# Optimization experiments

Measured on AMD Instinct MI355X. Metric: run time of the kernel, lower is better.

Reference implementation:

```python
import jax, jax.numpy as jnp
import numpy as np

N = 50000      # nodes
K = 15         # k_max candidate neighbors per node
D = 128        # node_dim
H = 64         # hidden_dim
K_MIN = 2.0
K_MAX = 15.0
TAU = 0.5      # edge_tau
LAM = 1.0      # selector_lambda


def setup_inputs() -> dict:
    key = jax.random.key(0)
    ks = jax.random.split(key, 16)
    x = jax.random.normal(ks[0], (N, D), dtype=jnp.float32)
    src = jax.random.randint(ks[1], (N * K,), 0, N)
    dst = jnp.repeat(jnp.arange(N), K)  # edges grouped by dst, as the module requires
    edge_index = jnp.stack([src, dst]).astype(jnp.int64)
    edge_dist = jax.random.uniform(ks[2], (N * K,), dtype=jnp.float32)

    def lin(k, fin, fout):
        return jax.random.normal(k, (fin, fout), dtype=jnp.float32) / np.sqrt(fin)

    EIN = 2 * D + 1  # edge MLP input: [x_dst, x_src, dist]
    return {
        "x": x, "edge_index": edge_index, "edge_dist": edge_dist,
        "ew1": lin(ks[3], EIN, H), "eb1": jnp.zeros((H,), jnp.float32),
        "ew2": lin(ks[4], H, H),   "eb2": jnp.zeros((H,), jnp.float32),
        "ew3": lin(ks[5], H, 1),   "eb3": jnp.zeros((1,), jnp.float32),
        "dw1": lin(ks[6], D + 1, H), "db1": jnp.zeros((H,), jnp.float32),
        "dw2": lin(ks[7], H, H),     "db2": jnp.zeros((H,), jnp.float32),
        "dw3": lin(ks[8], H, 1),     "db3": jnp.zeros((1,), jnp.float32),
    }


def reference(x, edge_index, edge_dist, ew1, eb1, ew2, eb2, ew3, eb3,
              dw1, db1, dw2, db2, dw3, db3):
    src_mat = edge_index[0].reshape(N, K)              # (N, K)
    x_src = x[src_mat]                                 # gather: (N, K, D)
    x_dst = jnp.broadcast_to(x[:, None, :], (N, K, D))
    edge_feat = jnp.concatenate([x_dst, x_src, edge_dist.reshape(N, K, 1)], axis=-1)

    # edge MLP -> logits (eval mode: no gumbel-logistic noise)
    h = jax.nn.relu(edge_feat @ ew1 + eb1)
    h = jax.nn.relu(h @ ew2 + eb2)
    edge_logits = (h @ ew3 + eb3)[..., 0]              # (N, K)
    edge_energy = jax.nn.sigmoid(edge_logits / TAU)

    # degree MLP -> continuous k per node
    degree_hint = edge_energy.sum(axis=1, keepdims=True)
    g = jax.nn.relu(jnp.concatenate([x, degree_hint], axis=1) @ dw1 + db1)
    g = jax.nn.relu(g @ dw2 + db2)
    k_raw = (g @ dw3 + db3)[:, 0]
    k_cont = K_MIN + (K_MAX - K_MIN) * jax.nn.sigmoid(k_raw)  # (N,)

    # per-node descending sort + straight-through top-k gate
    perm = jnp.argsort(-edge_energy, axis=1)
    energy_sorted = jnp.take_along_axis(edge_energy, perm, axis=1)
    ranks = jnp.arange(1, K + 1, dtype=x.dtype)[None, :]
    gate_soft = jax.nn.sigmoid((k_cont[:, None] - ranks) / LAM)
    k_int = jnp.clip(jnp.round(k_cont), K_MIN, K_MAX)
    gate_hard = (ranks <= k_int[:, None]).astype(gate_soft.dtype)
    gate = gate_soft + jax.lax.stop_gradient(gate_hard - gate_soft)

    gated_sorted = energy_sorted * gate
    inv_perm = jnp.argsort(perm, axis=1)               # undo the sort
    edge_gate = jnp.take_along_axis(gate, inv_perm, axis=1)
    edge_weight = jnp.take_along_axis(gated_sorted, inv_perm, axis=1)

    denom = jnp.maximum(edge_weight.sum(axis=1, keepdims=True), 1e-12)
    edge_weight = edge_weight / denom
    return (edge_weight.reshape(-1), edge_gate.reshape(-1),
            edge_energy.reshape(-1), k_cont)
```

## Files before the change

kernel.cpp:

```cpp
#include <hip/hip_runtime.h>
#include <cmath>

#define NN 50000
#define KK 15
#define DD 128
#define HH 64
#define NKE (NN * KK)

__global__ __launch_bounds__(256) void kP(const float* __restrict__ x,
                                          const float* __restrict__ ew1,
                                          const float* __restrict__ dw1,
                                          float* __restrict__ ws) {
    int lane = threadIdx.x & 63;
    int wv = __builtin_amdgcn_readfirstlane((int)(threadIdx.x >> 6));
    int r0 = blockIdx.x * 32 + wv * 8;
    if (r0 >= NN) return;

    const float* W0 = ew1;
    const float* W1 = ew1 + DD * HH;
    const float* W2 = dw1;
    const float* xw = x + (size_t)r0 * DD;

    float a0[8], a1[8], a2[8];
#pragma unroll
    for (int r = 0; r < 8; ++r) { a0[r] = 0.f; a1[r] = 0.f; a2[r] = 0.f; }

#pragma unroll 1
    for (int i4 = 0; i4 < DD / 4; ++i4) {
        float w00 = W0[(i4 * 4 + 0) * HH + lane];
        float w01 = W0[(i4 * 4 + 1) * HH + lane];
        float w02 = W0[(i4 * 4 + 2) * HH + lane];
        float w03 = W0[(i4 * 4 + 3) * HH + lane];
        float w10 = W1[(i4 * 4 + 0) * HH + lane];
        float w11 = W1[(i4 * 4 + 1) * HH + lane];
        float w12 = W1[(i4 * 4 + 2) * HH + lane];
        float w13 = W1[(i4 * 4 + 3) * HH + lane];
        float w20 = W2[(i4 * 4 + 0) * HH + lane];
        float w21 = W2[(i4 * 4 + 1) * HH + lane];
        float w22 = W2[(i4 * 4 + 2) * HH + lane];
        float w23 = W2[(i4 * 4 + 3) * HH + lane];
#pragma unroll
        for (int r = 0; r < 8; ++r) {
            float4 xv = *(const float4*)(xw + r * DD + i4 * 4);
            a0[r] = fmaf(xv.x, w00, a0[r]);
            a0[r] = fmaf(xv.y, w01, a0[r]);
            a0[r] = fmaf(xv.z, w02, a0[r]);
            a0[r] = fmaf(xv.w, w03, a0[r]);
            a1[r] = fmaf(xv.x, w10, a1[r]);
            a1[r] = fmaf(xv.y, w11, a1[r]);
            a1[r] = fmaf(xv.z, w12, a1[r]);
            a1[r] = fmaf(xv.w, w13, a1[r]);
            a2[r] = fmaf(xv.x, w20, a2[r]);
            a2[r] = fmaf(xv.y, w21, a2[r]);
            a2[r] = fmaf(xv.z, w22, a2[r]);
            a2[r] = fmaf(xv.w, w23, a2[r]);
        }
    }
    float* o0 = ws + (size_t)r0 * HH + lane;
    float* o1 = ws + (size_t)NN * HH + (size_t)r0 * HH + lane;
    float* o2 = ws + 2 * (size_t)NN * HH + (size_t)r0 * HH + lane;
#pragma unroll
    for (int r = 0; r < 8; ++r) {
        o0[r * HH] = a0[r];
        o1[r * HH] = a1[r];
        o2[r * HH] = a2[r];
    }
}

__global__ __launch_bounds__(128, 4) void kE(const int* __restrict__ srcIdx,
                                             const float* __restrict__ dist,
                                             const float* __restrict__ ws,
                                             const float* __restrict__ ew1,
                                             const float* __restrict__ eb1,
                                             const float* __restrict__ ew2,
                                             const float* __restrict__ eb2,
                                             const float* __restrict__ ew3,
                                             const float* __restrict__ eb3,
                                             float* __restrict__ energy_out) {
    int e = blockIdx.x * 128 + threadIdx.x;
    if (e >= NKE) return;
    int s = srcIdx[e];
    int d = e / KK;
    float dd = dist[e];
    const float* A = ws + (size_t)d * HH;
    const float* B = ws + (size_t)NN * HH + (size_t)s * HH;
    const float* w1l = ew1 + 2 * DD * HH;

    float acc[HH];
#pragma unroll
    for (int j = 0; j < HH; ++j) acc[j] = 0.f;

    float4 a4 = *(const float4*)A;
    float4 b4 = *(const float4*)B;
#pragma unroll 1
    for (int i4 = 0; i4 < HH / 4; ++i4) {
        float4 a = a4, b = b4;
        int nx = (i4 + 1 < HH / 4) ? (i4 + 1) : i4;
        a4 = *(const float4*)(A + nx * 4);
        b4 = *(const float4*)(B + nx * 4);
        float h[4];
        h[0] = fmaxf(a.x + b.x + dd * w1l[i4 * 4 + 0] + eb1[i4 * 4 + 0], 0.f);
        h[1] = fmaxf(a.y + b.y + dd * w1l[i4 * 4 + 1] + eb1[i4 * 4 + 1], 0.f);
        h[2] = fmaxf(a.z + b.z + dd * w1l[i4 * 4 + 2] + eb1[i4 * 4 + 2], 0.f);
        h[3] = fmaxf(a.w + b.w + dd * w1l[i4 * 4 + 3] + eb1[i4 * 4 + 3], 0.f);
#pragma unroll
        for (int k = 0; k < 4; ++k) {
            const float* wr = ew2 + (i4 * 4 + k) * HH;
#pragma unroll
            for (int j4 = 0; j4 < 16; ++j4) {
                float4 w = *(const float4*)(wr + j4 * 4);
                acc[j4 * 4 + 0] = fmaf(h[k], w.x, acc[j4 * 4 + 0]);
                acc[j4 * 4 + 1] = fmaf(h[k], w.y, acc[j4 * 4 + 1]);
                acc[j4 * 4 + 2] = fmaf(h[k], w.z, acc[j4 * 4 + 2]);
                acc[j4 * 4 + 3] = fmaf(h[k], w.w, acc[j4 * 4 + 3]);
            }
        }
    }
    float lg = eb3[0];
#pragma unroll
    for (int j = 0; j < HH; ++j)
        lg = fmaf(fmaxf(acc[j] + eb2[j], 0.f), ew3[j], lg);
    energy_out[e] = 1.f / (1.f + expf(-2.f * lg));
}

__global__ __launch_bounds__(128, 4) void kF(const float* __restrict__ ws,
                                             const float* __restrict__ dw1,
                                             const float* __restrict__ db1,
                                             const float* __restrict__ dw2,
                                             const float* __restrict__ db2,
                                             const float* __restrict__ dw3,
                                             const float* __restrict__ db3,
                                             float* __restrict__ out) {
    int n = blockIdx.x * 128 + threadIdx.x;
    if (n >= NN) return;
    const float* energy = out + 2 * (size_t)NKE;

    float ev[KK];
    float dh = 0.f;
#pragma unroll
    for (int j = 0; j < KK; ++j) {
        ev[j] = energy[(size_t)n * KK + j];
        dh += ev[j];
    }

    const float* XC = ws + 2 * (size_t)NN * HH + (size_t)n * HH;
    const float* w1l = dw1 + DD * HH;

    float acc[HH];
#pragma unroll
    for (int j = 0; j < HH; ++j) acc[j] = 0.f;

    float4 c4 = *(const float4*)XC;
#pragma unroll 1
    for (int i4 = 0; i4 < HH / 4; ++i4) {
        float4 c = c4;
        int nx = (i4 + 1 < HH / 4) ? (i4 + 1) : i4;
        c4 = *(const float4*)(XC + nx * 4);
        float cv[4] = {c.x, c.y, c.z, c.w};
#pragma unroll
        for (int m = 0; m < 4; ++m) {
            int k = i4 * 4 + m;
            float g = fmaxf(cv[m] + dh * w1l[k] + db1[k], 0.f);
            const float* wr = dw2 + k * HH;
#pragma unroll
            for (int j4 = 0; j4 < 16; ++j4) {
                float4 w = *(const float4*)(wr + j4 * 4);
                acc[j4 * 4 + 0] = fmaf(g, w.x, acc[j4 * 4 + 0]);
                acc[j4 * 4 + 1] = fmaf(g, w.y, acc[j4 * 4 + 1]);
                acc[j4 * 4 + 2] = fmaf(g, w.z, acc[j4 * 4 + 2]);
                acc[j4 * 4 + 3] = fmaf(g, w.w, acc[j4 * 4 + 3]);
            }
        }
    }
    float kraw = db3[0];
#pragma unroll
    for (int j = 0; j < HH; ++j)
        kraw = fmaf(fmaxf(acc[j] + db2[j], 0.f), dw3[j], kraw);

    float kcont = 2.f + 13.f / (1.f + expf(-kraw));
    out[3 * (size_t)NKE + n] = kcont;

    float se[16];
    int si[16];
#pragma unroll
    for (int j = 0; j < KK; ++j) { se[j] = ev[j]; si[j] = j; }
    se[15] = -1.f; si[15] = 15;

#pragma unroll
    for (int p = 1; p < 16; p <<= 1) {
#pragma unroll
        for (int k = p; k >= 1; k >>= 1) {
#pragma unroll
            for (int j = k & (p - 1); j + k < 16; j += 2 * k) {
#pragma unroll
                for (int i = 0; i < k; ++i) {
                    int a = i + j, b = i + j + k;
                    if (b < 16 && (a / (2 * p)) == (b / (2 * p))) {
                        bool sw = (se[b] > se[a]) ||
                                  (se[b] == se[a] && si[b] < si[a]);
                        float ea = sw ? se[b] : se[a];
                        float eb = sw ? se[a] : se[b];
                        int ia = sw ? si[b] : si[a];
                        int ib = sw ? si[a] : si[b];
                        se[a] = ea; se[b] = eb; si[a] = ia; si[b] = ib;
                    }
                }
            }
        }
    }

    float kint = rintf(kcont);
    kint = fminf(fmaxf(kint, 2.f), 15.f);

    float wsrt[KK];
    float denom = 0.f;
#pragma unroll
    for (int r = 0; r < KK; ++r) {
        float sel = ((float)(r + 1) <= kint) ? 1.f : 0.f;
        float wvv = se[r] * sel;
        wsrt[r] = wvv;
        denom += wvv;
    }
    denom = fmaxf(denom, 1e-12f);

#pragma unroll
    for (int r = 0; r < KK; ++r) {
        float sel = ((float)(r + 1) <= kint) ? 1.f : 0.f;
        int j0 = si[r];
        out[(size_t)NKE + (size_t)n * KK + j0] = sel;
        out[(size_t)n * KK + j0] = wsrt[r] / denom;
    }
}

extern "C" void kernel_launch(void* const* d_in, const int* in_sizes, int n_in,
                              void* d_out, int out_size, void* d_ws, size_t ws_size,
                              hipStream_t stream) {
    const float* x   = (const float*)d_in[0];
    const int*   ei  = (const int*)d_in[1];
    const float* ed  = (const float*)d_in[2];
    const float* ew1 = (const float*)d_in[3];
    const float* eb1 = (const float*)d_in[4];
    const float* ew2 = (const float*)d_in[5];
    const float* eb2 = (const float*)d_in[6];
    const float* ew3 = (const float*)d_in[7];
    const float* eb3 = (const float*)d_in[8];
    const float* dw1 = (const float*)d_in[9];
    const float* db1 = (const float*)d_in[10];
    const float* dw2 = (const float*)d_in[11];
    const float* db2 = (const float*)d_in[12];
    const float* dw3 = (const float*)d_in[13];
    const float* db3 = (const float*)d_in[14];
    float* out = (float*)d_out;
    float* ws  = (float*)d_ws;

    hipLaunchKernelGGL(kP, dim3((NN + 31) / 32), dim3(256), 0, stream,
                       x, ew1, dw1, ws);
    hipLaunchKernelGGL(kE, dim3((NKE + 127) / 128), dim3(128), 0, stream,
                       ei, ed, ws, ew1, eb1, ew2, eb2, ew3, eb3,
                       out + 2 * (size_t)NKE);
    hipLaunchKernelGGL(kF, dim3((NN + 127) / 128), dim3(128), 0, stream,
                       ws, dw1, db1, dw2, db2, dw3, db3, out);
}
```

Measured before the change: 269.8 us.

## Split edge and degree MLP hidden outputs across multiple threads per item

The edge MLP kernel now gives each edge to two lanes, each computing half of the 64 hidden outputs, and combines the partial logits with a shuffle. The degree/sort kernel uses four lanes per node, each computing 16 hidden outputs, reduces with shuffles, and spreads the output writes across the four lanes. The projection kernel also double-buffers its x row loads in registers. This cuts per-thread accumulator registers to raise occupancy and parallelism, at the cost of redundant first-layer work, duplicated sorts, and extra gather loads per edge.

```diff
diff --git a/kernel.cpp b/kernel.cpp
--- a/kernel.cpp
+++ b/kernel.cpp
@@ -25,37 +25,57 @@
 #pragma unroll
     for (int r = 0; r < 8; ++r) { a0[r] = 0.f; a1[r] = 0.f; a2[r] = 0.f; }
 
+    float4 xA[8], xB[8];
+#pragma unroll
+    for (int r = 0; r < 8; ++r) xA[r] = *(const float4*)(xw + r * DD);
+
+#define KP_STEP(I4, XB)                                                       \
+    {                                                                         \
+        float w00 = W0[((I4) * 4 + 0) * HH + lane];                           \
+        float w01 = W0[((I4) * 4 + 1) * HH + lane];                           \
+        float w02 = W0[((I4) * 4 + 2) * HH + lane];                           \
+        float w03 = W0[((I4) * 4 + 3) * HH + lane];                           \
+        float w10 = W1[((I4) * 4 + 0) * HH + lane];                           \
+        float w11 = W1[((I4) * 4 + 1) * HH + lane];                           \
+        float w12 = W1[((I4) * 4 + 2) * HH + lane];                           \
+        float w13 = W1[((I4) * 4 + 3) * HH + lane];                           \
+        float w20 = W2[((I4) * 4 + 0) * HH + lane];                           \
+        float w21 = W2[((I4) * 4 + 1) * HH + lane];                           \
+        float w22 = W2[((I4) * 4 + 2) * HH + lane];                           \
+        float w23 = W2[((I4) * 4 + 3) * HH + lane];                           \
+        _Pragma("unroll") for (int r = 0; r < 8; ++r) {                       \
+            float4 xv = XB[r];                                                \
+            a0[r] = fmaf(xv.x, w00, a0[r]);                                   \
+            a0[r] = fmaf(xv.y, w01, a0[r]);                                   \
+            a0[r] = fmaf(xv.z, w02, a0[r]);                                   \
+            a0[r] = fmaf(xv.w, w03, a0[r]);                                   \
+            a1[r] = fmaf(xv.x, w10, a1[r]);                                   \
+            a1[r] = fmaf(xv.y, w11, a1[r]);                                   \
+            a1[r] = fmaf(xv.z, w12, a1[r]);                                   \
+            a1[r] = fmaf(xv.w, w13, a1[r]);                                   \
+            a2[r] = fmaf(xv.x, w20, a2[r]);                                   \
+            a2[r] = fmaf(xv.y, w21, a2[r]);                                   \
+            a2[r] = fmaf(xv.z, w22, a2[r]);                                   \
+            a2[r] = fmaf(xv.w, w23, a2[r]);                                   \
+        }                                                                     \
+    }
+
 #pragma unroll 1
-    for (int i4 = 0; i4 < DD / 4; ++i4) {
-        float w00 = W0[(i4 * 4 + 0) * HH + lane];
-        float w01 = W0[(i4 * 4 + 1) * HH + lane];
-        float w02 = W0[(i4 * 4 + 2) * HH + lane];
-        float w03 = W0[(i4 * 4 + 3) * HH + lane];
-        float w10 = W1[(i4 * 4 + 0) * HH + lane];
-        float w11 = W1[(i4 * 4 + 1) * HH + lane];
-        float w12 = W1[(i4 * 4 + 2) * HH + lane];
-        float w13 = W1[(i4 * 4 + 3) * HH + lane];
-        float w20 = W2[(i4 * 4 + 0) * HH + lane];
-        float w21 = W2[(i4 * 4 + 1) * HH + lane];
-        float w22 = W2[(i4 * 4 + 2) * HH + lane];
-        float w23 = W2[(i4 * 4 + 3) * HH + lane];
-#pragma unroll
-        for (int r = 0; r < 8; ++r) {
-            float4 xv = *(const float4*)(xw + r * DD + i4 * 4);
-            a0[r] = fmaf(xv.x, w00, a0[r]);
-            a0[r] = fmaf(xv.y, w01, a0[r]);
-            a0[r] = fmaf(xv.z, w02, a0[r]);
-            a0[r] = fmaf(xv.w, w03, a0[r]);
-            a1[r] = fmaf(xv.x, w10, a1[r]);
-            a1[r] = fmaf(xv.y, w11, a1[r]);
-            a1[r] = fmaf(xv.z, w12, a1[r]);
-            a1[r] = fmaf(xv.w, w13, a1[r]);
-            a2[r] = fmaf(xv.x, w20, a2[r]);
-            a2[r] = fmaf(xv.y, w21, a2[r]);
-            a2[r] = fmaf(xv.z, w22, a2[r]);
-            a2[r] = fmaf(xv.w, w23, a2[r]);
-        }
-    }
+    for (int i2 = 0; i2 < 16; ++i2) {
+        int i4a = 2 * i2;
+        int i4b = 2 * i2 + 1;
+        int i4n = (i4b + 1 < 32) ? (i4b + 1) : i4b;
+#pragma unroll
+        for (int r = 0; r < 8; ++r)
+            xB[r] = *(const float4*)(xw + r * DD + i4b * 4);
+        KP_STEP(i4a, xA);
+#pragma unroll
+        for (int r = 0; r < 8; ++r)
+            xA[r] = *(const float4*)(xw + r * DD + i4n * 4);
+        KP_STEP(i4b, xB);
+    }
+#undef KP_STEP
+
     float* o0 = ws + (size_t)r0 * HH + lane;
     float* o1 = ws + (size_t)NN * HH + (size_t)r0 * HH + lane;
     float* o2 = ws + 2 * (size_t)NN * HH + (size_t)r0 * HH + lane;
@@ -67,7 +87,7 @@
     }
 }
 
-__global__ __launch_bounds__(128, 4) void kE(const int* __restrict__ srcIdx,
+__global__ __launch_bounds__(128, 6) void kE(const int* __restrict__ srcIdx,
                                              const float* __restrict__ dist,
                                              const float* __restrict__ ws,
                                              const float* __restrict__ ew1,
@@ -77,7 +97,9 @@
                                              const float* __restrict__ ew3,
                                              const float* __restrict__ eb3,
                                              float* __restrict__ energy_out) {
-    int e = blockIdx.x * 128 + threadIdx.x;
+    int t = blockIdx.x * 128 + threadIdx.x;
+    int e = t >> 1;
+    int jh = t & 1;
     if (e >= NKE) return;
     int s = srcIdx[e];
     int d = e / KK;
@@ -85,10 +107,11 @@
     const float* A = ws + (size_t)d * HH;
     const float* B = ws + (size_t)NN * HH + (size_t)s * HH;
     const float* w1l = ew1 + 2 * DD * HH;
-
-    float acc[HH];
-#pragma unroll
-    for (int j = 0; j < HH; ++j) acc[j] = 0.f;
+    const float* W2 = ew2 + jh * 32;
+
+    float acc[32];
+#pragma unroll
+    for (int j = 0; j < 32; ++j) acc[j] = 0.f;
 
     float4 a4 = *(const float4*)A;
     float4 b4 = *(const float4*)B;
@@ -105,9 +128,9 @@
         h[3] = fmaxf(a.w + b.w + dd * w1l[i4 * 4 + 3] + eb1[i4 * 4 + 3], 0.f);
 #pragma unroll
         for (int k = 0; k < 4; ++k) {
-            const float* wr = ew2 + (i4 * 4 + k) * HH;
-#pragma unroll
-            for (int j4 = 0; j4 < 16; ++j4) {
+            const float* wr = W2 + (i4 * 4 + k) * HH;
+#pragma unroll
+            for (int j4 = 0; j4 < 8; ++j4) {
                 float4 w = *(const float4*)(wr + j4 * 4);
                 acc[j4 * 4 + 0] = fmaf(h[k], w.x, acc[j4 * 4 + 0]);
                 acc[j4 * 4 + 1] = fmaf(h[k], w.y, acc[j4 * 4 + 1]);
@@ -116,14 +139,17 @@
             }
         }
     }
-    float lg = eb3[0];
-#pragma unroll
-    for (int j = 0; j < HH; ++j)
-        lg = fmaf(fmaxf(acc[j] + eb2[j], 0.f), ew3[j], lg);
-    energy_out[e] = 1.f / (1.f + expf(-2.f * lg));
-}
-
-__global__ __launch_bounds__(128, 4) void kF(const float* __restrict__ ws,
+    float lg = 0.f;
+#pragma unroll
+    for (int j = 0; j < 32; ++j)
+        lg = fmaf(fmaxf(acc[j] + eb2[jh * 32 + j], 0.f), ew3[jh * 32 + j], lg);
+    lg += __shfl_xor(lg, 1);
+    lg += eb3[0];
+    if (jh == 0)
+        energy_out[e] = 1.f / (1.f + expf(-2.f * lg));
+}
+
+__global__ __launch_bounds__(256, 3) void kF(const float* __restrict__ ws,
                                              const float* __restrict__ dw1,
                                              const float* __restrict__ db1,
                                              const float* __restrict__ dw2,
@@ -131,7 +157,9 @@
                                              const float* __restrict__ dw3,
                                              const float* __restrict__ db3,
                                              float* __restrict__ out) {
-    int n = blockIdx.x * 128 + threadIdx.x;
+    int t = blockIdx.x * 256 + threadIdx.x;
+    int n = t >> 2;
+    int p = t & 3;
     if (n >= NN) return;
     const float* energy = out + 2 * (size_t)NKE;
 
@@ -145,10 +173,11 @@
 
     const float* XC = ws + 2 * (size_t)NN * HH + (size_t)n * HH;
     const float* w1l = dw1 + DD * HH;
-
-    float acc[HH];
-#pragma unroll
-    for (int j = 0; j < HH; ++j) acc[j] = 0.f;
+    const float* W2 = dw2 + p * 16;
+
+    float acc[16];
+#pragma unroll
+    for (int j = 0; j < 16; ++j) acc[j] = 0.f;
 
     float4 c4 = *(const float4*)XC;
 #pragma unroll 1
@@ -161,9 +190,9 @@
         for (int m = 0; m < 4; ++m) {
             int k = i4 * 4 + m;
             float g = fmaxf(cv[m] + dh * w1l[k] + db1[k], 0.f);
-            const float* wr = dw2 + k * HH;
-#pragma unroll
-            for (int j4 = 0; j4 < 16; ++j4) {
+            const float* wr = W2 + k * HH;
+#pragma unroll
+            for (int j4 = 0; j4 < 4; ++j4) {
                 float4 w = *(const float4*)(wr + j4 * 4);
                 acc[j4 * 4 + 0] = fmaf(g, w.x, acc[j4 * 4 + 0]);
                 acc[j4 * 4 + 1] = fmaf(g, w.y, acc[j4 * 4 + 1]);
@@ -172,13 +201,16 @@
             }
         }
     }
-    float kraw = db3[0];
-#pragma unroll
-    for (int j = 0; j < HH; ++j)
-        kraw = fmaf(fmaxf(acc[j] + db2[j], 0.f), dw3[j], kraw);
+    float kp_ = 0.f;
+#pragma unroll
+    for (int j = 0; j < 16; ++j)
+        kp_ = fmaf(fmaxf(acc[j] + db2[p * 16 + j], 0.f), dw3[p * 16 + j], kp_);
+    kp_ += __shfl_xor(kp_, 1);
+    kp_ += __shfl_xor(kp_, 2);
+    float kraw = kp_ + db3[0];
 
     float kcont = 2.f + 13.f / (1.f + expf(-kraw));
-    out[3 * (size_t)NKE + n] = kcont;
+    if (p == 3) out[3 * (size_t)NKE + n] = kcont;
 
     float se[16];
     int si[16];
@@ -187,15 +219,15 @@
     se[15] = -1.f; si[15] = 15;
 
 #pragma unroll
-    for (int p = 1; p < 16; p <<= 1) {
-#pragma unroll
-        for (int k = p; k >= 1; k >>= 1) {
-#pragma unroll
-            for (int j = k & (p - 1); j + k < 16; j += 2 * k) {
+    for (int pp = 1; pp < 16; pp <<= 1) {
+#pragma unroll
+        for (int k = pp; k >= 1; k >>= 1) {
+#pragma unroll
+            for (int j = k & (pp - 1); j + k < 16; j += 2 * k) {
 #pragma unroll
                 for (int i = 0; i < k; ++i) {
                     int a = i + j, b = i + j + k;
-                    if (b < 16 && (a / (2 * p)) == (b / (2 * p))) {
+                    if (b < 16 && (a / (2 * pp)) == (b / (2 * pp))) {
                         bool sw = (se[b] > se[a]) ||
                                   (se[b] == se[a] && si[b] < si[a]);
                         float ea = sw ? se[b] : se[a];
@@ -225,10 +257,12 @@
 
 #pragma unroll
     for (int r = 0; r < KK; ++r) {
-        float sel = ((float)(r + 1) <= kint) ? 1.f : 0.f;
-        int j0 = si[r];
-        out[(size_t)NKE + (size_t)n * KK + j0] = sel;
-        out[(size_t)n * KK + j0] = wsrt[r] / denom;
+        if ((r & 3) == p) {
+            float sel = ((float)(r + 1) <= kint) ? 1.f : 0.f;
+            int j0 = si[r];
+            out[(size_t)NKE + (size_t)n * KK + j0] = sel;
+            out[(size_t)n * KK + j0] = wsrt[r] / denom;
+        }
     }
 }
 
@@ -255,9 +289,9 @@
 
     hipLaunchKernelGGL(kP, dim3((NN + 31) / 32), dim3(256), 0, stream,
                        x, ew1, dw1, ws);
-    hipLaunchKernelGGL(kE, dim3((NKE + 127) / 128), dim3(128), 0, stream,
+    hipLaunchKernelGGL(kE, dim3((2 * NKE + 127) / 128), dim3(128), 0, stream,
                        ei, ed, ws, ew1, eb1, ew2, eb2, ew3, eb3,
                        out + 2 * (size_t)NKE);
-    hipLaunchKernelGGL(kF, dim3((NN + 127) / 128), dim3(128), 0, stream,
+    hipLaunchKernelGGL(kF, dim3((4 * NN + 255) / 256), dim3(128 * 2), 0, stream,
                        ws, dw1, db1, dw2, db2, dw3, db3, out);
 }
```

After: 941.2 us. 3.49x slower.

## Split edge and degree MLP hidden outputs across multiple threads with shuffle reduction

Applied to the files above, without the earlier changes.

The edge MLP kernel now assigns two threads per edge, each computing half of the 64 second-layer outputs, and combines the partial logits with a lane shuffle. The degree/sort kernel uses four threads per node, each computing 16 hidden outputs, reduces with shuffles, and spreads the scattered output writes across the four lanes. This cuts per-thread register pressure and raises thread-level parallelism, in exchange for redundant loads and redundant sorting work per thread, plus twice as many threads for the edge stage.

```diff
diff --git a/kernel.cpp b/kernel.cpp
--- a/kernel.cpp
+++ b/kernel.cpp
@@ -77,7 +77,9 @@
                                              const float* __restrict__ ew3,
                                              const float* __restrict__ eb3,
                                              float* __restrict__ energy_out) {
-    int e = blockIdx.x * 128 + threadIdx.x;
+    int t = blockIdx.x * 128 + threadIdx.x;
+    int e = t >> 1;
+    int jh = t & 1;
     if (e >= NKE) return;
     int s = srcIdx[e];
     int d = e / KK;
@@ -85,10 +87,11 @@
     const float* A = ws + (size_t)d * HH;
     const float* B = ws + (size_t)NN * HH + (size_t)s * HH;
     const float* w1l = ew1 + 2 * DD * HH;
-
-    float acc[HH];
-#pragma unroll
-    for (int j = 0; j < HH; ++j) acc[j] = 0.f;
+    const float* W2 = ew2 + jh * 32;
+
+    float acc[32];
+#pragma unroll
+    for (int j = 0; j < 32; ++j) acc[j] = 0.f;
 
     float4 a4 = *(const float4*)A;
     float4 b4 = *(const float4*)B;
@@ -105,9 +108,9 @@
         h[3] = fmaxf(a.w + b.w + dd * w1l[i4 * 4 + 3] + eb1[i4 * 4 + 3], 0.f);
 #pragma unroll
         for (int k = 0; k < 4; ++k) {
-            const float* wr = ew2 + (i4 * 4 + k) * HH;
-#pragma unroll
-            for (int j4 = 0; j4 < 16; ++j4) {
+            const float* wr = W2 + (i4 * 4 + k) * HH;
+#pragma unroll
+            for (int j4 = 0; j4 < 8; ++j4) {
                 float4 w = *(const float4*)(wr + j4 * 4);
                 acc[j4 * 4 + 0] = fmaf(h[k], w.x, acc[j4 * 4 + 0]);
                 acc[j4 * 4 + 1] = fmaf(h[k], w.y, acc[j4 * 4 + 1]);
@@ -116,14 +119,17 @@
             }
         }
     }
-    float lg = eb3[0];
-#pragma unroll
-    for (int j = 0; j < HH; ++j)
-        lg = fmaf(fmaxf(acc[j] + eb2[j], 0.f), ew3[j], lg);
-    energy_out[e] = 1.f / (1.f + expf(-2.f * lg));
-}
-
-__global__ __launch_bounds__(128, 4) void kF(const float* __restrict__ ws,
+    float lg = 0.f;
+#pragma unroll
+    for (int j = 0; j < 32; ++j)
+        lg = fmaf(fmaxf(acc[j] + eb2[jh * 32 + j], 0.f), ew3[jh * 32 + j], lg);
+    lg += __shfl_xor(lg, 1);
+    lg += eb3[0];
+    if (jh == 0)
+        energy_out[e] = 1.f / (1.f + expf(-2.f * lg));
+}
+
+__global__ __launch_bounds__(256, 3) void kF(const float* __restrict__ ws,
                                              const float* __restrict__ dw1,
                                              const float* __restrict__ db1,
                                              const float* __restrict__ dw2,
@@ -131,7 +137,9 @@
                                              const float* __restrict__ dw3,
                                              const float* __restrict__ db3,
                                              float* __restrict__ out) {
-    int n = blockIdx.x * 128 + threadIdx.x;
+    int t = blockIdx.x * 256 + threadIdx.x;
+    int n = t >> 2;
+    int p = t & 3;
     if (n >= NN) return;
     const float* energy = out + 2 * (size_t)NKE;
 
@@ -145,10 +153,11 @@
 
     const float* XC = ws + 2 * (size_t)NN * HH + (size_t)n * HH;
     const float* w1l = dw1 + DD * HH;
-
-    float acc[HH];
-#pragma unroll
-    for (int j = 0; j < HH; ++j) acc[j] = 0.f;
+    const float* W2 = dw2 + p * 16;
+
+    float acc[16];
+#pragma unroll
+    for (int j = 0; j < 16; ++j) acc[j] = 0.f;
 
     float4 c4 = *(const float4*)XC;
 #pragma unroll 1
@@ -161,9 +170,9 @@
         for (int m = 0; m < 4; ++m) {
             int k = i4 * 4 + m;
             float g = fmaxf(cv[m] + dh * w1l[k] + db1[k], 0.f);
-            const float* wr = dw2 + k * HH;
-#pragma unroll
-            for (int j4 = 0; j4 < 16; ++j4) {
+            const float* wr = W2 + k * HH;
+#pragma unroll
+            for (int j4 = 0; j4 < 4; ++j4) {
                 float4 w = *(const float4*)(wr + j4 * 4);
                 acc[j4 * 4 + 0] = fmaf(g, w.x, acc[j4 * 4 + 0]);
                 acc[j4 * 4 + 1] = fmaf(g, w.y, acc[j4 * 4 + 1]);
@@ -172,13 +181,16 @@
             }
         }
     }
-    float kraw = db3[0];
-#pragma unroll
-    for (int j = 0; j < HH; ++j)
-        kraw = fmaf(fmaxf(acc[j] + db2[j], 0.f), dw3[j], kraw);
+    float kp_ = 0.f;
+#pragma unroll
+    for (int j = 0; j < 16; ++j)
+        kp_ = fmaf(fmaxf(acc[j] + db2[p * 16 + j], 0.f), dw3[p * 16 + j], kp_);
+    kp_ += __shfl_xor(kp_, 1);
+    kp_ += __shfl_xor(kp_, 2);
+    float kraw = kp_ + db3[0];
 
     float kcont = 2.f + 13.f / (1.f + expf(-kraw));
-    out[3 * (size_t)NKE + n] = kcont;
+    if (p == 3) out[3 * (size_t)NKE + n] = kcont;
 
     float se[16];
     int si[16];
@@ -187,15 +199,15 @@
     se[15] = -1.f; si[15] = 15;
 
 #pragma unroll
-    for (int p = 1; p < 16; p <<= 1) {
-#pragma unroll
-        for (int k = p; k >= 1; k >>= 1) {
-#pragma unroll
-            for (int j = k & (p - 1); j + k < 16; j += 2 * k) {
+    for (int pp = 1; pp < 16; pp <<= 1) {
+#pragma unroll
+        for (int k = pp; k >= 1; k >>= 1) {
+#pragma unroll
+            for (int j = k & (pp - 1); j + k < 16; j += 2 * k) {
 #pragma unroll
                 for (int i = 0; i < k; ++i) {
                     int a = i + j, b = i + j + k;
-                    if (b < 16 && (a / (2 * p)) == (b / (2 * p))) {
+                    if (b < 16 && (a / (2 * pp)) == (b / (2 * pp))) {
                         bool sw = (se[b] > se[a]) ||
                                   (se[b] == se[a] && si[b] < si[a]);
                         float ea = sw ? se[b] : se[a];
@@ -225,10 +237,12 @@
 
 #pragma unroll
     for (int r = 0; r < KK; ++r) {
-        float sel = ((float)(r + 1) <= kint) ? 1.f : 0.f;
-        int j0 = si[r];
-        out[(size_t)NKE + (size_t)n * KK + j0] = sel;
-        out[(size_t)n * KK + j0] = wsrt[r] / denom;
+        if ((r & 3) == p) {
+            float sel = ((float)(r + 1) <= kint) ? 1.f : 0.f;
+            int j0 = si[r];
+            out[(size_t)NKE + (size_t)n * KK + j0] = sel;
+            out[(size_t)n * KK + j0] = wsrt[r] / denom;
+        }
     }
 }
 
@@ -255,9 +269,9 @@
 
     hipLaunchKernelGGL(kP, dim3((NN + 31) / 32), dim3(256), 0, stream,
                        x, ew1, dw1, ws);
-    hipLaunchKernelGGL(kE, dim3((NKE + 127) / 128), dim3(128), 0, stream,
+    hipLaunchKernelGGL(kE, dim3((2 * NKE + 127) / 128), dim3(128), 0, stream,
                        ei, ed, ws, ew1, eb1, ew2, eb2, ew3, eb3,
                        out + 2 * (size_t)NKE);
-    hipLaunchKernelGGL(kF, dim3((NN + 127) / 128), dim3(128), 0, stream,
+    hipLaunchKernelGGL(kF, dim3((4 * NN + 255) / 256), dim3(256), 0, stream,
                        ws, dw1, db1, dw2, db2, dw3, db3, out);
 }
```

Result: slower. 913.0 us (+238.4%).
